# Performance work log

Hardware: AMD Instinct MI355X
Metric: run time of the kernel (lower is better)

Reference implementation:

```python
import jax, jax.numpy as jnp
import numpy as np

N_NODES = 131072
BATCH = 128
H = 256


def setup_inputs() -> dict:
    key = jax.random.key(0)
    k1, k2, k3, k4 = jax.random.split(key, 4)
    node_features = jax.random.normal(k1, (N_NODES, H), dtype=jnp.float32)
    # strictly increasing offsets (root indices) so no segment is empty
    offsets = jnp.sort(jax.random.randint(k2, (BATCH,), 0, N_NODES - BATCH)) + jnp.arange(BATCH)
    offsets = offsets.astype(jnp.int64)
    W1 = jax.random.normal(k3, (H, H), dtype=jnp.float32) / np.sqrt(H)
    b1 = jnp.zeros((H,), dtype=jnp.float32)
    W2 = jax.random.normal(k4, (H, 1), dtype=jnp.float32) / np.sqrt(H)
    b2 = jnp.zeros((1,), dtype=jnp.float32)
    return {"node_features": node_features, "offsets": offsets,
            "W1": W1, "b1": b1, "W2": W2, "b2": b2}


def _segment_bounds(offsets, n_nodes):
    # Faithful to the torch loop:
    #   i == 0       : [offsets[0],   offsets[1])
    #   0 < i < B-1  : [offsets[i-1], offsets[i+1])
    #   i == B-1     : [offsets[B-2], n_nodes)
    B = offsets.shape[0]
    starts = jnp.concatenate([offsets[:1], offsets[:-1]])          # (B,)
    ends = jnp.concatenate([offsets[2:], jnp.array([n_nodes, n_nodes], dtype=offsets.dtype)])
    if B == 1:
        starts = jnp.zeros((1,), offsets.dtype)
        ends = jnp.full((1,), n_nodes, offsets.dtype)
    return starts, ends


def reference(node_features, offsets, W1, b1, W2, b2):
    N = node_features.shape[0]
    # attention MLP scores for every node, computed once: (N,)
    scores = (jnp.tanh(node_features @ W1 + b1) @ W2 + b2)[:, 0]
    starts, ends = _segment_bounds(offsets, N)
    idx = jnp.arange(N)
    mask = (idx[None, :] >= starts[:, None]) & (idx[None, :] < ends[:, None])  # (B, N)
    logits = jnp.where(mask, scores[None, :], jnp.float32(-1e30))
    attn = jax.nn.softmax(logits, axis=1)              # (B, N), zero outside segment
    return attn @ node_features                        # (B, H)
```

## Files before the change

kernel.cpp:

```cpp
#include <hip/hip_runtime.h>
#include <hip/hip_bf16.h>

#define N_NODES 131072
#define BATCH 128
#define H 256
#define TROWS 32
#define NTILES (N_NODES / TROWS)

typedef _Float16 half8 __attribute__((ext_vector_type(8)));
typedef _Float16 half4 __attribute__((ext_vector_type(4)));
typedef float floatx4 __attribute__((ext_vector_type(4)));

__global__ __launch_bounds__(256) void prep_kernel(
    const float* __restrict__ W1, _Float16* __restrict__ W1p,
    float* __restrict__ pacc, float* __restrict__ pz)
{
    const int bid = blockIdx.x;
    const int tid = threadIdx.x;
    if (bid < 32) {
        const int g = bid * 256 + tid;
        const int ct = g >> 9;
        const int ks = (g >> 6) & 7;
        const int l  = g & 63;
        const int k0 = ks * 32 + (l >> 4) * 8;
        const int col = ct * 16 + (l & 15);
        half8 h;
        #pragma unroll
        for (int j = 0; j < 8; ++j) h[j] = (_Float16)W1[(k0 + j) * H + col];
        reinterpret_cast<half8*>(W1p)[g] = h;
    } else {
        pacc[(bid - 32) * 256 + tid] = 0.f;
        if (bid == 32 && tid < BATCH) pz[tid] = 0.f;
    }
}

__global__ __launch_bounds__(256, 7) void fused_kernel(
    const float* __restrict__ X, const _Float16* __restrict__ W1p,
    const float* __restrict__ b1, const float* __restrict__ W2,
    const float* __restrict__ b2, const int* __restrict__ offsets,
    float* __restrict__ pacc, float* __restrict__ pz)
{
    __shared__ __align__(16) _Float16 Xs[TROWS * H];
    __shared__ float sp[4][TROWS];
    __shared__ float scL[TROWS];
    __shared__ float accL[4][H];
    __shared__ float zLs[4];
    __shared__ int offL[BATCH];

    const int tid = threadIdx.x;
    const int wave = tid >> 6;
    const int lane = tid & 63;

    const int bid = (int)(blockIdx.x & 7) * (NTILES / 8) + (int)(blockIdx.x >> 3);
    const int t0 = bid * TROWS;

    if (tid < BATCH) offL[tid] = offsets[tid];

    {
        const float4* Xv = reinterpret_cast<const float4*>(X + (long long)t0 * H);
        #pragma unroll
        for (int i = 0; i < 4; ++i) {
            const int c = tid + i * 256;
            const int row = c >> 5;
            const int col8 = c & 31;
            float4 a  = Xv[row * 64 + col8 * 2];
            float4 bq = Xv[row * 64 + col8 * 2 + 1];
            half8 h;
            h[0] = (_Float16)a.x;  h[1] = (_Float16)a.y;
            h[2] = (_Float16)a.z;  h[3] = (_Float16)a.w;
            h[4] = (_Float16)bq.x; h[5] = (_Float16)bq.y;
            h[6] = (_Float16)bq.z; h[7] = (_Float16)bq.w;
            int byte = row * 512 + (col8 * 16 ^ ((row & 7) << 4));
            *reinterpret_cast<half8*>(reinterpret_cast<char*>(Xs) + byte) = h;
        }
    }
    __syncthreads();

    floatx4 acc[2][4];
    #pragma unroll
    for (int rt = 0; rt < 2; ++rt)
        #pragma unroll
        for (int ctl = 0; ctl < 4; ++ctl)
            acc[rt][ctl] = (floatx4){0.f, 0.f, 0.f, 0.f};

    const half8* Bw = reinterpret_cast<const half8*>(W1p) + wave * 2048 + lane;

    #pragma unroll 1
    for (int ks = 0; ks < 8; ++ks) {
        half8 bf0 = Bw[ks * 64];
        half8 bf1 = Bw[512 + ks * 64];
        half8 bf2 = Bw[1024 + ks * 64];
        half8 bf3 = Bw[1536 + ks * 64];
        half8 af[2];
        #pragma unroll
        for (int rt = 0; rt < 2; ++rt) {
            const int row = rt * 16 + (lane & 15);
            const int byte = row * 512 +
                ((ks * 64 + (lane >> 4) * 16) ^ ((row & 7) << 4));
            af[rt] = *reinterpret_cast<const half8*>(
                reinterpret_cast<const char*>(Xs) + byte);
        }
        #pragma unroll
        for (int rt = 0; rt < 2; ++rt) {
            acc[rt][0] = __builtin_amdgcn_mfma_f32_16x16x32_f16(af[rt], bf0, acc[rt][0], 0, 0, 0);
            acc[rt][1] = __builtin_amdgcn_mfma_f32_16x16x32_f16(af[rt], bf1, acc[rt][1], 0, 0, 0);
            acc[rt][2] = __builtin_amdgcn_mfma_f32_16x16x32_f16(af[rt], bf2, acc[rt][2], 0, 0, 0);
            acc[rt][3] = __builtin_amdgcn_mfma_f32_16x16x32_f16(af[rt], bf3, acc[rt][3], 0, 0, 0);
        }
    }

    float w2v[4], b1v[4];
    #pragma unroll
    for (int ctl = 0; ctl < 4; ++ctl) {
        const int col = wave * 64 + ctl * 16 + (lane & 15);
        w2v[ctl] = W2[col];
        b1v[ctl] = b1[col];
    }

    float sc[2][4];
    #pragma unroll
    for (int rt = 0; rt < 2; ++rt) {
        #pragma unroll
        for (int reg = 0; reg < 4; ++reg) {
            float s = 0.f;
            #pragma unroll
            for (int ctl = 0; ctl < 4; ++ctl) {
                const float x = acc[rt][ctl][reg] + b1v[ctl];
                const float t = 1.f - 2.f / (__expf(2.f * x) + 1.f);
                s = fmaf(t, w2v[ctl], s);
            }
            sc[rt][reg] = s;
        }
    }
    #pragma unroll
    for (int off = 1; off < 16; off <<= 1)
        #pragma unroll
        for (int rt = 0; rt < 2; ++rt)
            #pragma unroll
            for (int reg = 0; reg < 4; ++reg)
                sc[rt][reg] += __shfl_xor(sc[rt][reg], off);

    if ((lane & 15) == 0) {
        #pragma unroll
        for (int rt = 0; rt < 2; ++rt)
            #pragma unroll
            for (int reg = 0; reg < 4; ++reg)
                sp[wave][rt * 16 + (lane >> 4) * 4 + reg] = sc[rt][reg];
    }
    __syncthreads();
    if (tid < TROWS)
        scL[tid] = __expf(sp[0][tid] + sp[1][tid] + sp[2][tid] + sp[3][tid] + b2[0]);
    __syncthreads();

    int g_lo, g_hi;
    {
        int node = t0;
        if (node < offL[0]) g_lo = -1;
        else {
            int lo = 0, hi = BATCH - 1;
            while (lo < hi) { int mid = (lo + hi + 1) >> 1; if (offL[mid] <= node) lo = mid; else hi = mid - 1; }
            g_lo = lo;
        }
        node = t0 + TROWS - 1;
        if (node < offL[0]) g_hi = -1;
        else {
            int lo = 0, hi = BATCH - 1;
            while (lo < hi) { int mid = (lo + hi + 1) >> 1; if (offL[mid] <= node) lo = mid; else hi = mid - 1; }
            g_hi = lo;
        }
    }

    for (int g = (g_lo < 0 ? 0 : g_lo); g <= g_hi; ++g) {
        const int rs = max(t0, offL[g]);
        const int re = min(t0 + TROWS, (g == BATCH - 1) ? N_NODES : offL[g + 1]);

        float4 a4 = {0.f, 0.f, 0.f, 0.f};
        float z = 0.f;
        for (int i = rs + wave; i < re; i += 4) {
            const int r = i - t0;
            const float p = scL[r];
            const int byte = r * 512 + ((((lane >> 1) ^ (r & 7))) << 4) + (lane & 1) * 8;
            half4 xv = *reinterpret_cast<const half4*>(
                reinterpret_cast<const char*>(Xs) + byte);
            a4.x = fmaf(p, (float)xv[0], a4.x);
            a4.y = fmaf(p, (float)xv[1], a4.y);
            a4.z = fmaf(p, (float)xv[2], a4.z);
            a4.w = fmaf(p, (float)xv[3], a4.w);
            z += p;
        }
        reinterpret_cast<float4*>(&accL[wave][0])[lane] = a4;
        if (lane == 0) zLs[wave] = z;
        __syncthreads();
        const float v = accL[0][tid] + accL[1][tid] + accL[2][tid] + accL[3][tid];
        atomicAdd(&pacc[g * H + tid], v);
        if (tid == 0) atomicAdd(&pz[g], zLs[0] + zLs[1] + zLs[2] + zLs[3]);
        __syncthreads();
    }
}

__global__ __launch_bounds__(256) void reduce_kernel(
    const float* __restrict__ pacc, const float* __restrict__ pz,
    float* __restrict__ out)
{
    const int b = blockIdx.x;
    const int tid = threadIdx.x;
    const int g0 = (b == 0) ? 0 : b - 1;
    const int g1 = (b >= BATCH - 1) ? BATCH - 1 : b + 1;

    float r = 0.f, z = 0.f;
    for (int g = g0; g <= g1; ++g) {
        r += pacc[g * H + tid];
        z += pz[g];
    }
    out[b * H + tid] = r / z;
}

extern "C" void kernel_launch(void* const* d_in, const int* in_sizes, int n_in,
                              void* d_out, int out_size, void* d_ws, size_t ws_size,
                              hipStream_t stream)
{
    const float* X     = (const float*)d_in[0];
    const int* offs    = (const int*)d_in[1];
    const float* W1    = (const float*)d_in[2];
    const float* b1    = (const float*)d_in[3];
    const float* W2    = (const float*)d_in[4];
    const float* b2    = (const float*)d_in[5];
    float* out         = (float*)d_out;

    float* pacc   = (float*)d_ws;
    float* pz     = pacc + BATCH * H;
    _Float16* W1p = (_Float16*)(pz + BATCH);

    prep_kernel<<<160, 256, 0, stream>>>(W1, W1p, pacc, pz);
    fused_kernel<<<NTILES, 256, 0, stream>>>(X, W1p, b1, W2, b2, offs, pacc, pz);
    reduce_kernel<<<BATCH, 256, 0, stream>>>(pacc, pz, out);
}
```

Measured before the change: 61.02 us.

## Load X tiles directly into LDS as fp32 via global_load_lds

Replaces the register-staged fp32-to-fp16 conversion of the X tile with direct global-to-LDS async loads (global_load_lds, 16 bytes per lane) into an fp32 shared buffer with an XOR swizzle. The fp16 conversion moves to the MFMA operand read, and the weighted-sum stage now reads fp32 from LDS, which also avoids fp16 rounding of X in the pooled output. LDS use doubles to 32KB per block, so the occupancy hint drops from 7 to 4 blocks, and every MFMA step now does two LDS reads plus a conversion.

```diff
diff --git a/kernel.cpp b/kernel.cpp
--- a/kernel.cpp
+++ b/kernel.cpp
@@ -8,8 +8,10 @@
 #define NTILES (N_NODES / TROWS)
 
 typedef _Float16 half8 __attribute__((ext_vector_type(8)));
-typedef _Float16 half4 __attribute__((ext_vector_type(4)));
 typedef float floatx4 __attribute__((ext_vector_type(4)));
+
+typedef __attribute__((address_space(3))) void lds_void_t;
+typedef __attribute__((address_space(1))) const void gbl_void_t;
 
 __global__ __launch_bounds__(256) void prep_kernel(
     const float* __restrict__ W1, _Float16* __restrict__ W1p,
@@ -34,13 +36,13 @@
     }
 }
 
-__global__ __launch_bounds__(256, 7) void fused_kernel(
+__global__ __launch_bounds__(256, 4) void fused_kernel(
     const float* __restrict__ X, const _Float16* __restrict__ W1p,
     const float* __restrict__ b1, const float* __restrict__ W2,
     const float* __restrict__ b2, const int* __restrict__ offsets,
     float* __restrict__ pacc, float* __restrict__ pz)
 {
-    __shared__ __align__(16) _Float16 Xs[TROWS * H];
+    __shared__ __align__(16) float Xsf[TROWS * H];
     __shared__ float sp[4][TROWS];
     __shared__ float scL[TROWS];
     __shared__ float accL[4][H];
@@ -57,24 +59,17 @@
     if (tid < BATCH) offL[tid] = offsets[tid];
 
     {
-        const float4* Xv = reinterpret_cast<const float4*>(X + (long long)t0 * H);
-        #pragma unroll
-        for (int i = 0; i < 4; ++i) {
-            const int c = tid + i * 256;
-            const int row = c >> 5;
-            const int col8 = c & 31;
-            float4 a  = Xv[row * 64 + col8 * 2];
-            float4 bq = Xv[row * 64 + col8 * 2 + 1];
-            half8 h;
-            h[0] = (_Float16)a.x;  h[1] = (_Float16)a.y;
-            h[2] = (_Float16)a.z;  h[3] = (_Float16)a.w;
-            h[4] = (_Float16)bq.x; h[5] = (_Float16)bq.y;
-            h[6] = (_Float16)bq.z; h[7] = (_Float16)bq.w;
-            int byte = row * 512 + (col8 * 16 ^ ((row & 7) << 4));
-            *reinterpret_cast<half8*>(reinterpret_cast<char*>(Xs) + byte) = h;
+        #pragma unroll
+        for (int i = 0; i < 8; ++i) {
+            const int r = wave * 8 + i;
+            const float* g = X + ((long long)(t0 + r) << 8) + ((lane ^ (r & 7)) << 2);
+            __builtin_amdgcn_global_load_lds((gbl_void_t*)g,
+                                             (lds_void_t*)&Xsf[r * 256], 16, 0, 0);
         }
     }
     __syncthreads();
+
+    const float4* Xf4 = reinterpret_cast<const float4*>(Xsf);
 
     floatx4 acc[2][4];
     #pragma unroll
@@ -95,10 +90,16 @@
         #pragma unroll
         for (int rt = 0; rt < 2; ++rt) {
             const int row = rt * 16 + (lane & 15);
-            const int byte = row * 512 +
-                ((ks * 64 + (lane >> 4) * 16) ^ ((row & 7) << 4));
-            af[rt] = *reinterpret_cast<const half8*>(
-                reinterpret_cast<const char*>(Xs) + byte);
+            const int s = row & 7;
+            const int c0 = ks * 8 + (lane >> 4) * 2;
+            float4 x0 = Xf4[row * 64 + (c0 ^ s)];
+            float4 x1 = Xf4[row * 64 + ((c0 + 1) ^ s)];
+            half8 h;
+            h[0] = (_Float16)x0.x; h[1] = (_Float16)x0.y;
+            h[2] = (_Float16)x0.z; h[3] = (_Float16)x0.w;
+            h[4] = (_Float16)x1.x; h[5] = (_Float16)x1.y;
+            h[6] = (_Float16)x1.z; h[7] = (_Float16)x1.w;
+            af[rt] = h;
         }
         #pragma unroll
         for (int rt = 0; rt < 2; ++rt) {
@@ -179,13 +180,11 @@
         for (int i = rs + wave; i < re; i += 4) {
             const int r = i - t0;
             const float p = scL[r];
-            const int byte = r * 512 + ((((lane >> 1) ^ (r & 7))) << 4) + (lane & 1) * 8;
-            half4 xv = *reinterpret_cast<const half4*>(
-                reinterpret_cast<const char*>(Xs) + byte);
-            a4.x = fmaf(p, (float)xv[0], a4.x);
-            a4.y = fmaf(p, (float)xv[1], a4.y);
-            a4.z = fmaf(p, (float)xv[2], a4.z);
-            a4.w = fmaf(p, (float)xv[3], a4.w);
+            float4 xv = Xf4[r * 64 + (lane ^ (r & 7))];
+            a4.x = fmaf(p, xv.x, a4.x);
+            a4.y = fmaf(p, xv.y, a4.y);
+            a4.z = fmaf(p, xv.z, a4.z);
+            a4.w = fmaf(p, xv.w, a4.w);
             z += p;
         }
         reinterpret_cast<float4*>(&accL[wave][0])[lane] = a4;
```

Result: slower. 67.52 us (+10.7%).

## Process two 32-row tiles per block to halve block count

Applied to the files above, without the earlier changes.

Each block now loads 64 rows of X into two shared-memory tiles, then runs the MFMA score computation and the segment accumulation for both tiles in turn. Half as many blocks are launched, which cuts per-block overhead such as loading offsets and the b1/W2 fetch, and allows more X loads in flight per block. The cost is double the shared memory per block and a lower occupancy hint (4 instead of 7), so there may be less latency hiding across blocks.

```diff
diff --git a/kernel.cpp b/kernel.cpp
--- a/kernel.cpp
+++ b/kernel.cpp
@@ -3,9 +3,9 @@
 
 #define N_NODES 131072
 #define BATCH 128
+#define TROWS 32
 #define H 256
-#define TROWS 32
-#define NTILES (N_NODES / TROWS)
+#define NBLOCKS (N_NODES / 64)
 
 typedef _Float16 half8 __attribute__((ext_vector_type(8)));
 typedef _Float16 half4 __attribute__((ext_vector_type(4)));
@@ -34,15 +34,15 @@
     }
 }
 
-__global__ __launch_bounds__(256, 7) void fused_kernel(
+__global__ __launch_bounds__(256, 4) void fused_kernel(
     const float* __restrict__ X, const _Float16* __restrict__ W1p,
     const float* __restrict__ b1, const float* __restrict__ W2,
     const float* __restrict__ b2, const int* __restrict__ offsets,
     float* __restrict__ pacc, float* __restrict__ pz)
 {
-    __shared__ __align__(16) _Float16 Xs[TROWS * H];
-    __shared__ float sp[4][TROWS];
-    __shared__ float scL[TROWS];
+    __shared__ __align__(16) _Float16 Xs[2][TROWS * H];
+    __shared__ float sp[2][4][TROWS];
+    __shared__ float scL[2][TROWS];
     __shared__ float accL[4][H];
     __shared__ float zLs[4];
     __shared__ int offL[BATCH];
@@ -51,15 +51,16 @@
     const int wave = tid >> 6;
     const int lane = tid & 63;
 
-    const int bid = (int)(blockIdx.x & 7) * (NTILES / 8) + (int)(blockIdx.x >> 3);
-    const int t0 = bid * TROWS;
+    const int bid = (int)(blockIdx.x & 7) * (NBLOCKS / 8) + (int)(blockIdx.x >> 3);
+    const int t0a = bid * 64;
+    const int t0b = t0a + TROWS;
 
     if (tid < BATCH) offL[tid] = offsets[tid];
 
     {
-        const float4* Xv = reinterpret_cast<const float4*>(X + (long long)t0 * H);
-        #pragma unroll
-        for (int i = 0; i < 4; ++i) {
+        const float4* Xv = reinterpret_cast<const float4*>(X + (long long)t0a * H);
+        #pragma unroll
+        for (int i = 0; i < 8; ++i) {
             const int c = tid + i * 256;
             const int row = c >> 5;
             const int col8 = c & 31;
@@ -70,44 +71,13 @@
             h[2] = (_Float16)a.z;  h[3] = (_Float16)a.w;
             h[4] = (_Float16)bq.x; h[5] = (_Float16)bq.y;
             h[6] = (_Float16)bq.z; h[7] = (_Float16)bq.w;
-            int byte = row * 512 + (col8 * 16 ^ ((row & 7) << 4));
-            *reinterpret_cast<half8*>(reinterpret_cast<char*>(Xs) + byte) = h;
+            const int r = row & 31;
+            const int byte = r * 512 + (col8 * 16 ^ ((r & 7) << 4));
+            *reinterpret_cast<half8*>(
+                reinterpret_cast<char*>(&Xs[row >> 5][0]) + byte) = h;
         }
     }
     __syncthreads();
-
-    floatx4 acc[2][4];
-    #pragma unroll
-    for (int rt = 0; rt < 2; ++rt)
-        #pragma unroll
-        for (int ctl = 0; ctl < 4; ++ctl)
-            acc[rt][ctl] = (floatx4){0.f, 0.f, 0.f, 0.f};
-
-    const half8* Bw = reinterpret_cast<const half8*>(W1p) + wave * 2048 + lane;
-
-    #pragma unroll 1
-    for (int ks = 0; ks < 8; ++ks) {
-        half8 bf0 = Bw[ks * 64];
-        half8 bf1 = Bw[512 + ks * 64];
-        half8 bf2 = Bw[1024 + ks * 64];
-        half8 bf3 = Bw[1536 + ks * 64];
-        half8 af[2];
-        #pragma unroll
-        for (int rt = 0; rt < 2; ++rt) {
-            const int row = rt * 16 + (lane & 15);
-            const int byte = row * 512 +
-                ((ks * 64 + (lane >> 4) * 16) ^ ((row & 7) << 4));
-            af[rt] = *reinterpret_cast<const half8*>(
-                reinterpret_cast<const char*>(Xs) + byte);
-        }
-        #pragma unroll
-        for (int rt = 0; rt < 2; ++rt) {
-            acc[rt][0] = __builtin_amdgcn_mfma_f32_16x16x32_f16(af[rt], bf0, acc[rt][0], 0, 0, 0);
-            acc[rt][1] = __builtin_amdgcn_mfma_f32_16x16x32_f16(af[rt], bf1, acc[rt][1], 0, 0, 0);
-            acc[rt][2] = __builtin_amdgcn_mfma_f32_16x16x32_f16(af[rt], bf2, acc[rt][2], 0, 0, 0);
-            acc[rt][3] = __builtin_amdgcn_mfma_f32_16x16x32_f16(af[rt], bf3, acc[rt][3], 0, 0, 0);
-        }
-    }
 
     float w2v[4], b1v[4];
     #pragma unroll
@@ -117,84 +87,130 @@
         b1v[ctl] = b1[col];
     }
 
-    float sc[2][4];
+    const half8* Bw = reinterpret_cast<const half8*>(W1p) + wave * 2048 + lane;
+
     #pragma unroll
-    for (int rt = 0; rt < 2; ++rt) {
-        #pragma unroll
-        for (int reg = 0; reg < 4; ++reg) {
-            float s = 0.f;
-            #pragma unroll
-            for (int ctl = 0; ctl < 4; ++ctl) {
-                const float x = acc[rt][ctl][reg] + b1v[ctl];
-                const float t = 1.f - 2.f / (__expf(2.f * x) + 1.f);
-                s = fmaf(t, w2v[ctl], s);
-            }
-            sc[rt][reg] = s;
-        }
-    }
+    for (int tile = 0; tile < 2; ++tile) {
+        const char* Xb = reinterpret_cast<const char*>(&Xs[tile][0]);
+
+        floatx4 acc[2][4];
+        #pragma unroll
+        for (int rt = 0; rt < 2; ++rt)
+            #pragma unroll
+            for (int ctl = 0; ctl < 4; ++ctl)
+                acc[rt][ctl] = (floatx4){0.f, 0.f, 0.f, 0.f};
+
+        #pragma unroll 1
+        for (int ks = 0; ks < 8; ++ks) {
+            half8 bf0 = Bw[ks * 64];
+            half8 bf1 = Bw[512 + ks * 64];
+            half8 bf2 = Bw[1024 + ks * 64];
+            half8 bf3 = Bw[1536 + ks * 64];
+            half8 af[2];
+            #pragma unroll
+            for (int rt = 0; rt < 2; ++rt) {
+                const int row = rt * 16 + (lane & 15);
+                const int byte = row * 512 +
+                    ((ks * 64 + (lane >> 4) * 16) ^ ((row & 7) << 4));
+                af[rt] = *reinterpret_cast<const half8*>(Xb + byte);
+            }
+            #pragma unroll
+            for (int rt = 0; rt < 2; ++rt) {
+                acc[rt][0] = __builtin_amdgcn_mfma_f32_16x16x32_f16(af[rt], bf0, acc[rt][0], 0, 0, 0);
+                acc[rt][1] = __builtin_amdgcn_mfma_f32_16x16x32_f16(af[rt], bf1, acc[rt][1], 0, 0, 0);
+                acc[rt][2] = __builtin_amdgcn_mfma_f32_16x16x32_f16(af[rt], bf2, acc[rt][2], 0, 0, 0);
+                acc[rt][3] = __builtin_amdgcn_mfma_f32_16x16x32_f16(af[rt], bf3, acc[rt][3], 0, 0, 0);
+            }
+        }
+
+        float sc[2][4];
+        #pragma unroll
+        for (int rt = 0; rt < 2; ++rt) {
+            #pragma unroll
+            for (int reg = 0; reg < 4; ++reg) {
+                float s = 0.f;
+                #pragma unroll
+                for (int ctl = 0; ctl < 4; ++ctl) {
+                    const float x = acc[rt][ctl][reg] + b1v[ctl];
+                    const float t = 1.f - 2.f / (__expf(2.f * x) + 1.f);
+                    s = fmaf(t, w2v[ctl], s);
+                }
+                sc[rt][reg] = s;
+            }
+        }
+        #pragma unroll
+        for (int off = 1; off < 16; off <<= 1)
+            #pragma unroll
+            for (int rt = 0; rt < 2; ++rt)
+                #pragma unroll
+                for (int reg = 0; reg < 4; ++reg)
+                    sc[rt][reg] += __shfl_xor(sc[rt][reg], off);
+
+        if ((lane & 15) == 0) {
+            #pragma unroll
+            for (int rt = 0; rt < 2; ++rt)
+                #pragma unroll
+                for (int reg = 0; reg < 4; ++reg)
+                    sp[tile][wave][rt * 16 + (lane >> 4) * 4 + reg] = sc[rt][reg];
+        }
+    }
+    __syncthreads();
+    if (tid < 64) {
+        const int tile = tid >> 5;
+        const int rr = tid & 31;
+        scL[tile][rr] = __expf(sp[tile][0][rr] + sp[tile][1][rr] +
+                               sp[tile][2][rr] + sp[tile][3][rr] + b2[0]);
+    }
+    __syncthreads();
+
     #pragma unroll
-    for (int off = 1; off < 16; off <<= 1)
-        #pragma unroll
-        for (int rt = 0; rt < 2; ++rt)
-            #pragma unroll
-            for (int reg = 0; reg < 4; ++reg)
-                sc[rt][reg] += __shfl_xor(sc[rt][reg], off);
-
-    if ((lane & 15) == 0) {
-        #pragma unroll
-        for (int rt = 0; rt < 2; ++rt)
-            #pragma unroll
-            for (int reg = 0; reg < 4; ++reg)
-                sp[wave][rt * 16 + (lane >> 4) * 4 + reg] = sc[rt][reg];
-    }
-    __syncthreads();
-    if (tid < TROWS)
-        scL[tid] = __expf(sp[0][tid] + sp[1][tid] + sp[2][tid] + sp[3][tid] + b2[0]);
-    __syncthreads();
-
-    int g_lo, g_hi;
-    {
-        int node = t0;
-        if (node < offL[0]) g_lo = -1;
-        else {
-            int lo = 0, hi = BATCH - 1;
-            while (lo < hi) { int mid = (lo + hi + 1) >> 1; if (offL[mid] <= node) lo = mid; else hi = mid - 1; }
-            g_lo = lo;
-        }
-        node = t0 + TROWS - 1;
-        if (node < offL[0]) g_hi = -1;
-        else {
-            int lo = 0, hi = BATCH - 1;
-            while (lo < hi) { int mid = (lo + hi + 1) >> 1; if (offL[mid] <= node) lo = mid; else hi = mid - 1; }
-            g_hi = lo;
-        }
-    }
-
-    for (int g = (g_lo < 0 ? 0 : g_lo); g <= g_hi; ++g) {
-        const int rs = max(t0, offL[g]);
-        const int re = min(t0 + TROWS, (g == BATCH - 1) ? N_NODES : offL[g + 1]);
-
-        float4 a4 = {0.f, 0.f, 0.f, 0.f};
-        float z = 0.f;
-        for (int i = rs + wave; i < re; i += 4) {
-            const int r = i - t0;
-            const float p = scL[r];
-            const int byte = r * 512 + ((((lane >> 1) ^ (r & 7))) << 4) + (lane & 1) * 8;
-            half4 xv = *reinterpret_cast<const half4*>(
-                reinterpret_cast<const char*>(Xs) + byte);
-            a4.x = fmaf(p, (float)xv[0], a4.x);
-            a4.y = fmaf(p, (float)xv[1], a4.y);
-            a4.z = fmaf(p, (float)xv[2], a4.z);
-            a4.w = fmaf(p, (float)xv[3], a4.w);
-            z += p;
-        }
-        reinterpret_cast<float4*>(&accL[wave][0])[lane] = a4;
-        if (lane == 0) zLs[wave] = z;
-        __syncthreads();
-        const float v = accL[0][tid] + accL[1][tid] + accL[2][tid] + accL[3][tid];
-        atomicAdd(&pacc[g * H + tid], v);
-        if (tid == 0) atomicAdd(&pz[g], zLs[0] + zLs[1] + zLs[2] + zLs[3]);
-        __syncthreads();
+    for (int tile = 0; tile < 2; ++tile) {
+        const int t0 = tile ? t0b : t0a;
+        const char* Xb = reinterpret_cast<const char*>(&Xs[tile][0]);
+
+        int g_lo, g_hi;
+        {
+            int node = t0;
+            if (node < offL[0]) g_lo = -1;
+            else {
+                int lo = 0, hi = BATCH - 1;
+                while (lo < hi) { int mid = (lo + hi + 1) >> 1; if (offL[mid] <= node) lo = mid; else hi = mid - 1; }
+                g_lo = lo;
+            }
+            node = t0 + TROWS - 1;
+            if (node < offL[0]) g_hi = -1;
+            else {
+                int lo = 0, hi = BATCH - 1;
+                while (lo < hi) { int mid = (lo + hi + 1) >> 1; if (offL[mid] <= node) lo = mid; else hi = mid - 1; }
+                g_hi = lo;
+            }
+        }
+
+        for (int g = (g_lo < 0 ? 0 : g_lo); g <= g_hi; ++g) {
+            const int rs = max(t0, offL[g]);
+            const int re = min(t0 + TROWS, (g == BATCH - 1) ? N_NODES : offL[g + 1]);
+
+            float4 a4 = {0.f, 0.f, 0.f, 0.f};
+            float z = 0.f;
+            for (int i = rs + wave; i < re; i += 4) {
+                const int r = i - t0;
+                const float p = scL[tile][r];
+                const int byte = r * 512 + ((((lane >> 1) ^ (r & 7))) << 4) + (lane & 1) * 8;
+                half4 xv = *reinterpret_cast<const half4*>(Xb + byte);
+                a4.x = fmaf(p, (float)xv[0], a4.x);
+                a4.y = fmaf(p, (float)xv[1], a4.y);
+                a4.z = fmaf(p, (float)xv[2], a4.z);
+                a4.w = fmaf(p, (float)xv[3], a4.w);
+                z += p;
+            }
+            reinterpret_cast<float4*>(&accL[wave][0])[lane] = a4;
+            if (lane == 0) zLs[wave] = z;
+            __syncthreads();
+            const float v = accL[0][tid] + accL[1][tid] + accL[2][tid] + accL[3][tid];
+            atomicAdd(&pacc[g * H + tid], v);
+            if (tid == 0) atomicAdd(&pz[g], zLs[0] + zLs[1] + zLs[2] + zLs[3]);
+            __syncthreads();
+        }
     }
 }
 
@@ -232,6 +248,6 @@
     _Float16* W1p = (_Float16*)(pz + BATCH);
 
     prep_kernel<<<160, 256, 0, stream>>>(W1, W1p, pacc, pz);
-    fused_kernel<<<NTILES, 256, 0, stream>>>(X, W1p, b1, W2, b2, offs, pacc, pz);
+    fused_kernel<<<NBLOCKS, 256, 0, stream>>>(X, W1p, b1, W2, b2, offs, pacc, pz);
     reduce_kernel<<<BATCH, 256, 0, stream>>>(pacc, pz, out);
 }
```

New measurement: 65.20 us. 6.9% more time.
